# Performance work log

Hardware: AMD Instinct MI355X
Metric: run time of the kernel (lower is better)

## Reference

```python
import jax, jax.numpy as jnp
import numpy as np

NUM_E = 100000
NUM_REL2 = 460  # 2 * num_rel
H = 200
N_EDGES = 1000000
B = 512
RRELU_SLOPE = (1.0 / 8.0 + 1.0 / 3.0) / 2.0  # F.rrelu eval-mode slope
BN_EPS = 1e-5


def setup_inputs() -> dict:
    key = jax.random.key(0)
    ks = jax.random.split(key, 20)
    d = {}
    d["ent_emb"] = jax.random.normal(ks[0], (NUM_E, H), jnp.float32) * 0.1
    d["rel_emb"] = jax.random.normal(ks[1], (NUM_REL2, H), jnp.float32) * 0.1
    d["W_neigh1"] = jax.random.normal(ks[2], (H, H), jnp.float32) * (1.0 / np.sqrt(H))
    d["W_loop1"] = jax.random.normal(ks[3], (H, H), jnp.float32) * (1.0 / np.sqrt(H))
    d["W_neigh2"] = jax.random.normal(ks[4], (H, H), jnp.float32) * (1.0 / np.sqrt(H))
    d["W_loop2"] = jax.random.normal(ks[5], (H, H), jnp.float32) * (1.0 / np.sqrt(H))
    d["gate_theta"] = jax.random.normal(ks[6], (NUM_E, H), jnp.float32) * 0.1
    d["gate_w"] = jax.random.normal(ks[7], (H, 1), jnp.float32) * (1.0 / np.sqrt(H))
    d["gate_b"] = jnp.zeros((1,), jnp.float32)
    d["bn_gamma"] = jnp.ones((3,), jnp.float32)
    d["bn_beta"] = jnp.zeros((3,), jnp.float32)
    d["conv_w"] = jax.random.normal(ks[8], (3,), jnp.float32)
    d["conv_b"] = jnp.zeros((1,), jnp.float32)
    d["freq"] = jax.random.normal(ks[9], (B, H), jnp.float32)
    d["src"] = jax.random.randint(ks[10], (N_EDGES,), 0, NUM_E, jnp.int64)
    d["dst"] = jax.random.randint(ks[11], (N_EDGES,), 0, NUM_E, jnp.int64)
    d["etype"] = jax.random.randint(ks[12], (N_EDGES,), 0, NUM_REL2, jnp.int64)
    d["s_idx"] = jax.random.randint(ks[13], (B,), 0, NUM_E, jnp.int64)
    d["r_idx"] = jax.random.randint(ks[14], (B,), 0, NUM_REL2, jnp.int64)
    return d


def _rrelu(x):
    return jnp.where(x >= 0, x, x * RRELU_SLOPE)


def _union_rgcn_layer(h, rel, W_neigh, W_loop, src, dst):
    # gather -> transform -> scatter (UnionRGCNLayer msg: (h_src + r_etype) @ W_neigh)
    msg = (h[src] + rel) @ W_neigh                      # [E, H]
    agg = jax.ops.segment_sum(msg, dst, num_segments=NUM_E)
    deg = jax.ops.segment_sum(jnp.ones((msg.shape[0],), h.dtype), dst, num_segments=NUM_E)
    agg = agg / jnp.maximum(deg, 1.0)[:, None]          # in-degree norm
    return _rrelu(agg + h @ W_loop)                     # self-loop + activation (dropout off, eval)


def reference(ent_emb, rel_emb, W_neigh1, W_loop1, W_neigh2, W_loop2,
              gate_theta, gate_w, gate_b, bn_gamma, bn_beta, conv_w, conv_b,
              freq, src, dst, etype, s_idx, r_idx):
    rel_per_edge = rel_emb[etype]                       # [E, H]
    # RGCNCell: 2 UnionRGCN layers
    h = _union_rgcn_layer(ent_emb, rel_per_edge, W_neigh1, W_loop1, src, dst)
    h = _union_rgcn_layer(h, rel_per_edge, W_neigh2, W_loop2, src, dst)
    # GatingMechanism: gate = sigmoid(linear(gate_theta[ids])); blend evolved vs static
    gate = jax.nn.sigmoid(gate_theta @ gate_w + gate_b)  # [N, 1]
    h_final = gate * h + (1.0 - gate) * ent_emb          # [N, H]
    # ConvE fusion: stack (entity, rel, frequency) as 3 channels
    e = h_final[s_idx]                                   # [B, H]
    r = rel_emb[r_idx]                                   # [B, H]
    x = jnp.stack([e, r, freq], axis=1)                  # [B, 3, H]
    # BatchNorm1d(3), batch statistics over (B, H) per channel
    mean = jnp.mean(x, axis=(0, 2), keepdims=True)
    var = jnp.var(x, axis=(0, 2), keepdims=True)
    x = (x - mean) * jax.lax.rsqrt(var + BN_EPS)
    x = x * bn_gamma[None, :, None] + bn_beta[None, :, None]
    x = jax.nn.relu(x)
    # Conv1d(3 -> 1, kernel_size=1): weighted channel sum
    q = jnp.einsum('bch,c->bh', x, conv_w) + conv_b      # [B, H]
    # score against all (evolved) entity embeddings
    scores = q @ h_final.T                               # [B, N]
    return scores
```

## Files before the change

### kernel.cpp

```cpp
#include <hip/hip_runtime.h>

#define N_ENT 100000
#define HDIM  200
#define NEDGE 1000000
#define BDIM  512
#define KPAD  416
#define NPAD  208
#define HPAD  224
#define SCAN_TILE 1024
#define SCAN_NB   ((N_ENT + SCAN_TILE - 1)/SCAN_TILE)
#define BN_NB 32

typedef short  short8v __attribute__((ext_vector_type(8)));
typedef float  float4v __attribute__((ext_vector_type(4)));

__device__ __forceinline__ float rrelu_f(float v){
    const float slope = (1.0f/8.0f + 1.0f/3.0f)*0.5f;
    return v >= 0.f ? v : v*slope;
}
__device__ __forceinline__ unsigned short f2bf(float f){
    unsigned int x = __float_as_uint(f);
    unsigned int r = (x + 0x7fffu + ((x >> 16) & 1u)) >> 16;
    return (unsigned short)r;
}
__device__ __forceinline__ float bf2f(unsigned short u){
    return __uint_as_float(((unsigned int)u) << 16);
}

__global__ void hist_k(const int* __restrict__ dst, int* __restrict__ deg){
    int e = blockIdx.x*blockDim.x + threadIdx.x;
    if (e < NEDGE) atomicAdd(&deg[dst[e]], 1);
}

__global__ __launch_bounds__(256) void scan_part_k(const int* __restrict__ deg, int* __restrict__ partial){
    int t = threadIdx.x;
    int base = blockIdx.x*SCAN_TILE + t*4;
    int s = 0;
    if (base + 3 < N_ENT){
        int4 v = *(const int4*)(deg + base);
        s = v.x + v.y + v.z + v.w;
    } else {
        for (int i=0;i<4;i++) if (base+i < N_ENT) s += deg[base+i];
    }
    #pragma unroll
    for (int off=32; off>=1; off>>=1) s += __shfl_xor(s, off);
    __shared__ int ws[4];
    if ((t&63)==0) ws[t>>6] = s;
    __syncthreads();
    if (t==0) partial[blockIdx.x] = ws[0]+ws[1]+ws[2]+ws[3];
}

__global__ void scan_mid_k(int* __restrict__ partial){
    __shared__ int sh[128];
    int t = threadIdx.x;
    int v = (t < SCAN_NB) ? partial[t] : 0;
    sh[t] = v;
    __syncthreads();
    for (int off=1; off<128; off<<=1){
        int u = (t>=off) ? sh[t-off] : 0;
        __syncthreads();
        sh[t] += u;
        __syncthreads();
    }
    if (t < SCAN_NB) partial[t] = sh[t] - v;
}

__global__ __launch_bounds__(256) void scan_fin_k(const int* __restrict__ deg, const int* __restrict__ partial,
        int* __restrict__ row_off, int* __restrict__ fill_pos){
    int t = threadIdx.x;
    int lane = t & 63;
    int base = blockIdx.x*SCAN_TILE + t*4;
    int v0=0,v1=0,v2=0,v3=0;
    if (base+3 < N_ENT){
        int4 v = *(const int4*)(deg + base);
        v0=v.x; v1=v.y; v2=v.z; v3=v.w;
    } else {
        if (base   < N_ENT) v0 = deg[base];
        if (base+1 < N_ENT) v1 = deg[base+1];
        if (base+2 < N_ENT) v2 = deg[base+2];
        if (base+3 < N_ENT) v3 = deg[base+3];
    }
    int s = v0+v1+v2+v3;
    int inc = s;
    #pragma unroll
    for (int off=1; off<64; off<<=1){
        int u = __shfl_up(inc, off);
        if (lane >= off) inc += u;
    }
    __shared__ int wsum[4];
    if (lane==63) wsum[t>>6] = inc;
    __syncthreads();
    int w = t>>6;
    int woff = 0;
    for (int i=0;i<w;i++) woff += wsum[i];
    int exc = partial[blockIdx.x] + woff + inc - s;
    int r0 = exc, r1 = exc+v0, r2 = exc+v0+v1, r3 = exc+v0+v1+v2;
    if (base+3 < N_ENT){
        *(int4*)(row_off+base)  = make_int4(r0,r1,r2,r3);
        *(int4*)(fill_pos+base) = make_int4(r0,r1,r2,r3);
    } else {
        if (base   < N_ENT){ row_off[base]  =r0; fill_pos[base]  =r0; }
        if (base+1 < N_ENT){ row_off[base+1]=r1; fill_pos[base+1]=r1; }
        if (base+2 < N_ENT){ row_off[base+2]=r2; fill_pos[base+2]=r2; }
        if (base+3 < N_ENT){ row_off[base+3]=r3; fill_pos[base+3]=r3; }
    }
    if (blockIdx.x==0 && t==0) row_off[N_ENT] = NEDGE;
}

__global__ void fill_k(const int* __restrict__ src, const int* __restrict__ dst, const int* __restrict__ et,
                       int* __restrict__ fill_pos, int2* __restrict__ cs){
    int e = blockIdx.x*blockDim.x + threadIdx.x;
    if (e < NEDGE){
        int p = atomicAdd(&fill_pos[dst[e]], 1);
        cs[p] = make_int2(src[e], et[e]);
    }
}

__global__ __launch_bounds__(256) void prep_ent_k(const float* __restrict__ ent,
        unsigned short* __restrict__ A1, unsigned short* __restrict__ A2){
    int w = threadIdx.x >> 6, l = threadIdx.x & 63;
    int n = blockIdx.x*4 + w;
    if (l < 50){
        float4 v = *(const float4*)(ent + (size_t)n*HDIM + 4*l);
        ushort4 o; o.x=f2bf(v.x); o.y=f2bf(v.y); o.z=f2bf(v.z); o.w=f2bf(v.w);
        *(ushort4*)(A1 + (size_t)n*KPAD + NPAD + 4*l) = o;
    }
    if (l < 8){
        A1[(size_t)n*KPAD + 200 + l] = 0; A1[(size_t)n*KPAD + 408 + l] = 0;
        A2[(size_t)n*KPAD + 200 + l] = 0; A2[(size_t)n*KPAD + 408 + l] = 0;
    }
}

__global__ void prep_rel_k(const float* __restrict__ rel, unsigned short* __restrict__ relb){
    int i = blockIdx.x*blockDim.x + threadIdx.x;
    if (i < 460*HDIM) relb[i] = f2bf(rel[i]);
}

__global__ void pack_w_k(const float* __restrict__ Wn, const float* __restrict__ Wl,
                         unsigned short* __restrict__ Bpack){
    int i = blockIdx.x*blockDim.x + threadIdx.x;
    if (i >= 13*13*64*8) return;
    int j = i & 7, l = (i >> 3) & 63, rest = i >> 9;
    int f = rest % 13, ks = rest / 13;
    int k = ks*32 + ((l >> 4) << 3) + j;
    int c = f*16 + (l & 15);
    float v = 0.f;
    if (c < HDIM){
        if (k < 200)                  v = Wn[(size_t)k*HDIM + c];
        else if (k >= 208 && k < 408) v = Wl[(size_t)(k-208)*HDIM + c];
    }
    Bpack[i] = f2bf(v);
}

__global__ __launch_bounds__(256) void spmm1_k(unsigned short* __restrict__ Apack,
        const unsigned short* __restrict__ relb,
        const int2* __restrict__ cs,
        const int* __restrict__ row_off,
        unsigned short* __restrict__ relavg){
    int wv = (blockIdx.x*256 + threadIdx.x) >> 6;
    int l = threadIdx.x & 63;
    if (l >= 50) return;
    int beg = row_off[wv], end = row_off[wv+1];
    const int el = 4*l;
    float x0=0.f,x1=0.f,x2=0.f,x3=0.f;
    float r0=0.f,r1=0.f,r2=0.f,r3=0.f;
    int e = beg;
    for (; e+4 <= end; e+=4){
        int2 c0 = cs[e], c1 = cs[e+1], c2 = cs[e+2], c3 = cs[e+3];
        ushort4 xa = *(const ushort4*)(Apack + (size_t)c0.x*KPAD + NPAD + el);
        ushort4 xb = *(const ushort4*)(Apack + (size_t)c1.x*KPAD + NPAD + el);
        ushort4 xc = *(const ushort4*)(Apack + (size_t)c2.x*KPAD + NPAD + el);
        ushort4 xd = *(const ushort4*)(Apack + (size_t)c3.x*KPAD + NPAD + el);
        ushort4 ra = *(const ushort4*)(relb + (size_t)c0.y*HDIM + el);
        ushort4 rb = *(const ushort4*)(relb + (size_t)c1.y*HDIM + el);
        ushort4 rc = *(const ushort4*)(relb + (size_t)c2.y*HDIM + el);
        ushort4 rd = *(const ushort4*)(relb + (size_t)c3.y*HDIM + el);
        x0 += bf2f(xa.x)+bf2f(xb.x)+bf2f(xc.x)+bf2f(xd.x);
        x1 += bf2f(xa.y)+bf2f(xb.y)+bf2f(xc.y)+bf2f(xd.y);
        x2 += bf2f(xa.z)+bf2f(xb.z)+bf2f(xc.z)+bf2f(xd.z);
        x3 += bf2f(xa.w)+bf2f(xb.w)+bf2f(xc.w)+bf2f(xd.w);
        r0 += bf2f(ra.x)+bf2f(rb.x)+bf2f(rc.x)+bf2f(rd.x);
        r1 += bf2f(ra.y)+bf2f(rb.y)+bf2f(rc.y)+bf2f(rd.y);
        r2 += bf2f(ra.z)+bf2f(rb.z)+bf2f(rc.z)+bf2f(rd.z);
        r3 += bf2f(ra.w)+bf2f(rb.w)+bf2f(rc.w)+bf2f(rd.w);
    }
    for (; e<end; e++){
        int2 c0 = cs[e];
        ushort4 xa = *(const ushort4*)(Apack + (size_t)c0.x*KPAD + NPAD + el);
        ushort4 ra = *(const ushort4*)(relb + (size_t)c0.y*HDIM + el);
        x0 += bf2f(xa.x); x1 += bf2f(xa.y); x2 += bf2f(xa.z); x3 += bf2f(xa.w);
        r0 += bf2f(ra.x); r1 += bf2f(ra.y); r2 += bf2f(ra.z); r3 += bf2f(ra.w);
    }
    float id = 1.f / fmaxf((float)(end-beg), 1.f);
    float g0 = r0*id, g1 = r1*id, g2 = r2*id, g3 = r3*id;
    ushort4 rv; rv.x=f2bf(g0); rv.y=f2bf(g1); rv.z=f2bf(g2); rv.w=f2bf(g3);
    *(ushort4*)(relavg + (size_t)wv*HDIM + el) = rv;
    ushort4 o;
    o.x=f2bf(x0*id+g0); o.y=f2bf(x1*id+g1); o.z=f2bf(x2*id+g2); o.w=f2bf(x3*id+g3);
    *(ushort4*)(Apack + (size_t)wv*KPAD + el) = o;
}

__global__ __launch_bounds__(256) void spmm2_k(unsigned short* __restrict__ Apack,
        const unsigned short* __restrict__ relavg,
        const int2* __restrict__ cs,
        const int* __restrict__ row_off){
    int wv = (blockIdx.x*256 + threadIdx.x) >> 6;
    int l = threadIdx.x & 63;
    if (l >= 50) return;
    int beg = row_off[wv], end = row_off[wv+1];
    const int el = 4*l;
    float x0=0.f,x1=0.f,x2=0.f,x3=0.f;
    int e = beg;
    for (; e+4 <= end; e+=4){
        int2 c0 = cs[e], c1 = cs[e+1], c2 = cs[e+2], c3 = cs[e+3];
        ushort4 xa = *(const ushort4*)(Apack + (size_t)c0.x*KPAD + NPAD + el);
        ushort4 xb = *(const ushort4*)(Apack + (size_t)c1.x*KPAD + NPAD + el);
        ushort4 xc = *(const ushort4*)(Apack + (size_t)c2.x*KPAD + NPAD + el);
        ushort4 xd = *(const ushort4*)(Apack + (size_t)c3.x*KPAD + NPAD + el);
        x0 += bf2f(xa.x)+bf2f(xb.x)+bf2f(xc.x)+bf2f(xd.x);
        x1 += bf2f(xa.y)+bf2f(xb.y)+bf2f(xc.y)+bf2f(xd.y);
        x2 += bf2f(xa.z)+bf2f(xb.z)+bf2f(xc.z)+bf2f(xd.z);
        x3 += bf2f(xa.w)+bf2f(xb.w)+bf2f(xc.w)+bf2f(xd.w);
    }
    for (; e<end; e++){
        int2 c0 = cs[e];
        ushort4 xa = *(const ushort4*)(Apack + (size_t)c0.x*KPAD + NPAD + el);
        x0 += bf2f(xa.x); x1 += bf2f(xa.y); x2 += bf2f(xa.z); x3 += bf2f(xa.w);
    }
    float id = 1.f / fmaxf((float)(end-beg), 1.f);
    ushort4 rv = *(const ushort4*)(relavg + (size_t)wv*HDIM + el);
    ushort4 o;
    o.x=f2bf(x0*id+bf2f(rv.x)); o.y=f2bf(x1*id+bf2f(rv.y));
    o.z=f2bf(x2*id+bf2f(rv.z)); o.w=f2bf(x3*id+bf2f(rv.w));
    *(ushort4*)(Apack + (size_t)wv*KPAD + el) = o;
}

__global__ __launch_bounds__(256) void gate_k(const float* __restrict__ th, const float* __restrict__ gw,
                       const float* __restrict__ gb, float* __restrict__ gate){
    int wv = (blockIdx.x*256 + threadIdx.x)>>6;
    int lane = threadIdx.x & 63;
    const float* t = th + (size_t)wv*HDIM;
    float s = t[lane]*gw[lane] + t[64+lane]*gw[64+lane] + t[128+lane]*gw[128+lane];
    if (lane<8) s += t[192+lane]*gw[192+lane];
    #pragma unroll
    for (int off=32; off>=1; off>>=1) s += __shfl_xor(s, off);
    if (lane==0) gate[wv] = 1.f/(1.f + expf(-(s + gb[0])));
}

template<int EPI>
__global__ __launch_bounds__(256,2) void gemm_layer_mfma_k(
        const unsigned short* __restrict__ Apack,
        const unsigned short* __restrict__ Bpack,
        unsigned short* __restrict__ OutB,
        const float* __restrict__ gate, const float* __restrict__ ent){
    __shared__ unsigned short OutS[128*208];
    const int tid = threadIdx.x;
    const int l   = tid & 63;
    const int w   = tid >> 6;
    const int n0  = blockIdx.x * 128;
    const int lr  = l & 15;
    const int lg  = l >> 4;
    int r0 = n0 + w*32 + lr;
    int r1 = r0 + 16;
    int c0 = r0 < N_ENT ? r0 : N_ENT-1;
    int c1 = r1 < N_ENT ? r1 : N_ENT-1;
    const unsigned short* ar0 = Apack + (size_t)c0*KPAD + lg*8;
    const unsigned short* ar1 = Apack + (size_t)c1*KPAD + lg*8;
    float4v acc[2][13];
    #pragma unroll
    for (int f=0; f<13; f++){
        acc[0][f] = (float4v){0.f,0.f,0.f,0.f};
        acc[1][f] = (float4v){0.f,0.f,0.f,0.f};
    }
    short8v a0 = *(const short8v*)(ar0);
    short8v a1 = *(const short8v*)(ar1);
    for (int ks=0; ks<13; ks++){
        short8v na0 = a0, na1 = a1;
        if (ks < 12){
            na0 = *(const short8v*)(ar0 + (ks+1)*32);
            na1 = *(const short8v*)(ar1 + (ks+1)*32);
        }
        const unsigned short* bp = Bpack + ((size_t)(ks*13)*64 + l)*8;
        #pragma unroll
        for (int f=0; f<13; f++){
            short8v b = *(const short8v*)(bp + (size_t)f*512);
            acc[0][f] = __builtin_amdgcn_mfma_f32_16x16x32_bf16(a0, b, acc[0][f], 0, 0, 0);
            acc[1][f] = __builtin_amdgcn_mfma_f32_16x16x32_bf16(a1, b, acc[1][f], 0, 0, 0);
        }
        a0 = na0; a1 = na1;
    }
    #pragma unroll
    for (int f=0; f<13; f++){
        int c = f*16 + lr;
        if (c < HDIM){
            #pragma unroll
            for (int j=0; j<4; j++){
                OutS[(w*32 + lg*4 + j)*208 + c]      = f2bf(rrelu_f(acc[0][f][j]));
                OutS[(w*32 + 16 + lg*4 + j)*208 + c] = f2bf(rrelu_f(acc[1][f][j]));
            }
        }
    }
    __syncthreads();
    for (int i = tid; i < 128*25; i += 256){
        int r = i/25, seg = i - r*25;
        int n = n0 + r;
        if (n >= N_ENT) continue;
        short8v v = *(const short8v*)(&OutS[r*208 + seg*8]);
        if (EPI == 2){
            float g = gate[n];
            const float4* ef = (const float4*)(ent + (size_t)n*HDIM + seg*8);
            float4 e0 = ef[0], e1 = ef[1];
            float ev[8] = {e0.x,e0.y,e0.z,e0.w,e1.x,e1.y,e1.z,e1.w};
            short8v o;
            #pragma unroll
            for (int j=0; j<8; j++){
                float x = g*bf2f((unsigned short)v[j]) + (1.f-g)*ev[j];
                o[j] = (short)f2bf(x);
            }
            *(short8v*)(OutB + (size_t)n*HPAD + seg*8) = o;
        } else {
            *(short8v*)(OutB + (size_t)n*KPAD + NPAD + seg*8) = v;
        }
    }
}

__global__ void zero_hfb_pad_k(unsigned short* __restrict__ hfb){
    int i = blockIdx.x*blockDim.x + threadIdx.x;
    if (i >= N_ENT*24) return;
    int n = i / 24, c = 200 + (i - n*24);
    hfb[(size_t)n*HPAD + c] = 0;
}

__global__ __launch_bounds__(256) void bn_part_k(const unsigned short* __restrict__ hfb,
        const float* __restrict__ rel, const float* __restrict__ freq,
        const int* __restrict__ s_idx, const int* __restrict__ r_idx,
        float* __restrict__ bnpart){
    int t = threadIdx.x;
    float acc[6] = {0,0,0,0,0,0};
    for (int i = blockIdx.x*256 + t; i < BDIM*HDIM; i += BN_NB*256){
        int b = i/HDIM, h = i - b*HDIM;
        float e = bf2f(hfb[(size_t)s_idx[b]*HPAD + h]);
        float r = rel[(size_t)r_idx[b]*HDIM + h];
        float f = freq[i];
        acc[0]+=e; acc[1]+=e*e; acc[2]+=r; acc[3]+=r*r; acc[4]+=f; acc[5]+=f*f;
    }
    __shared__ float red[4][6];
    #pragma unroll
    for (int c=0;c<6;c++){
        float s = acc[c];
        #pragma unroll
        for (int off=32; off>=1; off>>=1) s += __shfl_xor(s, off);
        if ((t&63)==0) red[t>>6][c] = s;
    }
    __syncthreads();
    if (t==0){
        #pragma unroll
        for (int c=0;c<6;c++)
            bnpart[blockIdx.x*6+c] = red[0][c]+red[1][c]+red[2][c]+red[3][c];
    }
}

__global__ void bn_fin_k(const float* __restrict__ bnpart, float* __restrict__ bnp){
    int t = threadIdx.x;
    if (t < 3){
        float s=0.f, q=0.f;
        for (int b=0;b<BN_NB;b++){ s += bnpart[b*6+2*t]; q += bnpart[b*6+2*t+1]; }
        const float inv = 1.f/(float)(BDIM*HDIM);
        float mean = s*inv;
        float var  = q*inv - mean*mean;
        bnp[t]   = mean;
        bnp[3+t] = rsqrtf(var + 1e-5f);
    }
}

__global__ void qt_k(const unsigned short* __restrict__ hfb, const float* __restrict__ rel,
        const float* __restrict__ freq, const int* __restrict__ s_idx, const int* __restrict__ r_idx,
        const float* __restrict__ gamma, const float* __restrict__ beta,
        const float* __restrict__ convw, const float* __restrict__ convb,
        const float* __restrict__ bnp, unsigned short* __restrict__ qb){
    int i = blockIdx.x*blockDim.x + threadIdx.x;
    if (i >= BDIM*HPAD) return;
    int b = i/HPAD, h = i - b*HPAD;
    if (h >= HDIM){ qb[i] = 0; return; }
    float x0 = bf2f(hfb[(size_t)s_idx[b]*HPAD + h]);
    float x1 = rel[(size_t)r_idx[b]*HDIM + h];
    float x2 = freq[(size_t)b*HDIM + h];
    float v0 = fmaxf((x0-bnp[0])*bnp[3]*gamma[0] + beta[0], 0.f);
    float v1 = fmaxf((x1-bnp[1])*bnp[4]*gamma[1] + beta[1], 0.f);
    float v2 = fmaxf((x2-bnp[2])*bnp[5]*gamma[2] + beta[2], 0.f);
    float q = v0*convw[0] + v1*convw[1] + v2*convw[2] + convb[0];
    qb[(size_t)b*HPAD + h] = f2bf(q);
}

__global__ __launch_bounds__(256,2) void scores_mfma_k(
        const unsigned short* __restrict__ hfb,
        const unsigned short* __restrict__ qb,
        float* __restrict__ out){
    const int tid = threadIdx.x;
    const int l   = tid & 63;
    const int w   = tid >> 6;
    const int lr  = l & 15;
    const int lg  = l >> 4;
    const int n0  = blockIdx.x * 64;
    float4v acc[8][4];
    #pragma unroll
    for (int bf=0; bf<8; bf++)
        #pragma unroll
        for (int nf=0; nf<4; nf++) acc[bf][nf] = (float4v){0,0,0,0};
    const unsigned short* hptr[4];
    #pragma unroll
    for (int nf=0; nf<4; nf++){
        int n = n0 + nf*16 + lr;
        if (n >= N_ENT) n = N_ENT-1;
        hptr[nf] = hfb + (size_t)n*HPAD + lg*8;
    }
    const unsigned short* qrow = qb + (size_t)(w*128 + lr)*HPAD + lg*8;
    for (int ks=0; ks<7; ks++){
        short8v hv[4];
        #pragma unroll
        for (int nf=0; nf<4; nf++) hv[nf] = *(const short8v*)(hptr[nf] + ks*32);
        #pragma unroll
        for (int bf=0; bf<8; bf++){
            short8v q = *(const short8v*)(qrow + (size_t)bf*16*HPAD + ks*32);
            #pragma unroll
            for (int nf=0; nf<4; nf++)
                acc[bf][nf] = __builtin_amdgcn_mfma_f32_16x16x32_bf16(q, hv[nf], acc[bf][nf], 0, 0, 0);
        }
    }
    #pragma unroll
    for (int bf=0; bf<8; bf++){
        int b = w*128 + bf*16 + lg*4;
        #pragma unroll
        for (int nf=0; nf<4; nf++){
            int n = n0 + nf*16 + lr;
            if (n >= N_ENT) continue;
            #pragma unroll
            for (int j=0; j<4; j++){
                out[(size_t)(b+j)*N_ENT + n] = acc[bf][nf][j];
            }
        }
    }
}

extern "C" void kernel_launch(void* const* d_in, const int* in_sizes, int n_in,
                              void* d_out, int out_size, void* d_ws, size_t ws_size,
                              hipStream_t stream) {
    const float* ent    = (const float*)d_in[0];
    const float* rel    = (const float*)d_in[1];
    const float* Wn1    = (const float*)d_in[2];
    const float* Wl1    = (const float*)d_in[3];
    const float* Wn2    = (const float*)d_in[4];
    const float* Wl2    = (const float*)d_in[5];
    const float* gtheta = (const float*)d_in[6];
    const float* gw     = (const float*)d_in[7];
    const float* gb     = (const float*)d_in[8];
    const float* gamma  = (const float*)d_in[9];
    const float* beta   = (const float*)d_in[10];
    const float* convw  = (const float*)d_in[11];
    const float* convb  = (const float*)d_in[12];
    const float* freq   = (const float*)d_in[13];
    const int*   src    = (const int*)d_in[14];
    const int*   dst    = (const int*)d_in[15];
    const int*   etype  = (const int*)d_in[16];
    const int*   s_idx  = (const int*)d_in[17];
    const int*   r_idx  = (const int*)d_in[18];
    float* out = (float*)d_out;

    char* ws = (char*)d_ws;
    size_t off = 0;
    auto alloc = [&](size_t bytes)->char*{
        char* p = ws + off;
        off += (bytes + 511) & ~(size_t)511;
        return p;
    };
    int*   deg      = (int*)alloc((size_t)N_ENT*4);
    int*   row_off  = (int*)alloc((size_t)(N_ENT+1)*4);
    int*   fill_pos = (int*)alloc((size_t)N_ENT*4);
    int*   partial  = (int*)alloc((size_t)SCAN_NB*4);
    int2*  cs       = (int2*)alloc((size_t)NEDGE*8);
    unsigned short* A1     = (unsigned short*)alloc((size_t)N_ENT*KPAD*2);
    unsigned short* A2     = (unsigned short*)alloc((size_t)N_ENT*KPAD*2);
    unsigned short* relavg = (unsigned short*)alloc((size_t)N_ENT*HDIM*2);
    unsigned short* relb   = (unsigned short*)alloc((size_t)460*HDIM*2);
    unsigned short* Bp1    = (unsigned short*)alloc((size_t)13*13*64*8*2);
    unsigned short* Bp2    = (unsigned short*)alloc((size_t)13*13*64*8*2);
    unsigned short* qb     = (unsigned short*)alloc((size_t)BDIM*HPAD*2);
    float* gate   = (float*)alloc((size_t)N_ENT*4);
    float* bnpart = (float*)alloc((size_t)BN_NB*6*4);
    float* bnp    = (float*)alloc(64);
    unsigned short* hfb = A1;

    hipMemsetAsync(deg, 0, (size_t)N_ENT*4, stream);

    const int EB = (NEDGE + 255)/256;
    hist_k<<<EB,256,0,stream>>>(dst, deg);
    scan_part_k<<<SCAN_NB,256,0,stream>>>(deg, partial);
    scan_mid_k<<<1,128,0,stream>>>(partial);
    scan_fin_k<<<SCAN_NB,256,0,stream>>>(deg, partial, row_off, fill_pos);
    fill_k<<<EB,256,0,stream>>>(src, dst, etype, fill_pos, cs);

    prep_ent_k<<<N_ENT/4,256,0,stream>>>(ent, A1, A2);
    prep_rel_k<<<(460*HDIM+255)/256,256,0,stream>>>(rel, relb);
    pack_w_k<<<(13*13*64*8+255)/256,256,0,stream>>>(Wn1, Wl1, Bp1);
    pack_w_k<<<(13*13*64*8+255)/256,256,0,stream>>>(Wn2, Wl2, Bp2);

    const int NWB = N_ENT/4;
    const int GTB = (N_ENT + 127)/128;

    spmm1_k<<<NWB,256,0,stream>>>(A1, relb, cs, row_off, relavg);
    gemm_layer_mfma_k<1><<<GTB,256,0,stream>>>(A1, Bp1, A2, nullptr, nullptr);

    zero_hfb_pad_k<<<(N_ENT*24+255)/256,256,0,stream>>>(hfb);
    gate_k<<<NWB,256,0,stream>>>(gtheta, gw, gb, gate);

    spmm2_k<<<NWB,256,0,stream>>>(A2, relavg, cs, row_off);
    gemm_layer_mfma_k<2><<<GTB,256,0,stream>>>(A2, Bp2, hfb, gate, ent);

    bn_part_k<<<BN_NB,256,0,stream>>>(hfb, rel, freq, s_idx, r_idx, bnpart);
    bn_fin_k<<<1,64,0,stream>>>(bnpart, bnp);
    qt_k<<<(BDIM*HPAD+255)/256,256,0,stream>>>(hfb, rel, freq, s_idx, r_idx, gamma, beta, convw, convb, bnp, qb);

    scores_mfma_k<<<(N_ENT+63)/64,256,0,stream>>>(hfb, qb, out);

    (void)in_sizes; (void)n_in; (void)out_size; (void)ws_size;
}
```

Measured before the change: 627.8 us.

## Split packed activation buffer into separate padded X/P buffers and fuse prep kernels

New measurement: 574.3 us. -8.5%, faster.

```diff
diff --git a/kernel.cpp b/kernel.cpp
--- a/kernel.cpp
+++ b/kernel.cpp
@@ -4,12 +4,14 @@
 #define HDIM  200
 #define NEDGE 1000000
 #define BDIM  512
-#define KPAD  416
-#define NPAD  208
-#define HPAD  224
+#define PITCH 224
+#define NSEG  28
+#define NF    13
 #define SCAN_TILE 1024
 #define SCAN_NB   ((N_ENT + SCAN_TILE - 1)/SCAN_TILE)
 #define BN_NB 32
+#define RELB_ELEMS (460*PITCH)
+#define BP_ELEMS   (14*NF*64*8)
 
 typedef short  short8v __attribute__((ext_vector_type(8)));
 typedef float  float4v __attribute__((ext_vector_type(4)));
@@ -25,6 +27,73 @@
 }
 __device__ __forceinline__ float bf2f(unsigned short u){
     return __uint_as_float(((unsigned int)u) << 16);
+}
+
+__device__ __forceinline__ void pack_b(int b, const float* __restrict__ Wn,
+        const float* __restrict__ Wl, unsigned short* __restrict__ Bp){
+    int i = b*1024 + threadIdx.x*4;
+    #pragma unroll
+    for (int k=0;k<4;k++){
+        int idx = i+k;
+        if (idx < BP_ELEMS){
+            int j = idx & 7, l = (idx >> 3) & 63, rest = idx >> 9;
+            int f = rest % NF, ks = rest / NF;
+            int kk = ks*32 + ((l >> 4) << 3) + j;
+            int c  = f*16 + (l & 15);
+            float v = 0.f;
+            if (c < HDIM){
+                if (kk < 200)                  v = Wn[(size_t)kk*HDIM + c];
+                else if (kk >= 224 && kk < 424) v = Wl[(size_t)(kk-224)*HDIM + c];
+            }
+            Bp[idx] = f2bf(v);
+        }
+    }
+}
+
+__global__ __launch_bounds__(256) void init_k(const float* __restrict__ ent,
+        const float* __restrict__ rel,
+        const float* __restrict__ Wn1, const float* __restrict__ Wl1,
+        const float* __restrict__ Wn2, const float* __restrict__ Wl2,
+        int* __restrict__ deg, unsigned short* __restrict__ relb,
+        unsigned short* __restrict__ Bp1, unsigned short* __restrict__ Bp2,
+        unsigned short* __restrict__ Xbuf1){
+    int b = blockIdx.x;
+    if (b < 98){
+        int i = b*1024 + threadIdx.x*4;
+        if (i+3 < N_ENT) *(int4*)(deg+i) = make_int4(0,0,0,0);
+        else { for (int k=0;k<4;k++) if (i+k < N_ENT) deg[i+k]=0; }
+        return;
+    }
+    b -= 98;
+    if (b < 101){
+        int i = b*1024 + threadIdx.x*4;
+        #pragma unroll
+        for (int k=0;k<4;k++){
+            int idx = i+k;
+            if (idx < RELB_ELEMS){
+                int r = idx / PITCH, c = idx - r*PITCH;
+                relb[idx] = (c < HDIM) ? f2bf(rel[(size_t)r*HDIM + c]) : 0;
+            }
+        }
+        return;
+    }
+    b -= 101;
+    if (b < 91){ pack_b(b, Wn1, Wl1, Bp1); return; }
+    b -= 91;
+    if (b < 91){ pack_b(b, Wn2, Wl2, Bp2); return; }
+    b -= 91;
+    int w = threadIdx.x >> 6, l = threadIdx.x & 63;
+    if (l >= 56) return;
+    int n = b*4 + w;
+    int el = 4*l;
+    ushort4 o;
+    if (el < HDIM){
+        float4 v = *(const float4*)(ent + (size_t)n*HDIM + el);
+        o.x=f2bf(v.x); o.y=f2bf(v.y); o.z=f2bf(v.z); o.w=f2bf(v.w);
+    } else {
+        o.x=o.y=o.z=o.w=0;
+    }
+    *(ushort4*)(Xbuf1 + (size_t)n*PITCH + el) = o;
 }
 
 __global__ void hist_k(const int* __restrict__ dst, int* __restrict__ deg){
@@ -116,50 +185,15 @@
     }
 }
 
-__global__ __launch_bounds__(256) void prep_ent_k(const float* __restrict__ ent,
-        unsigned short* __restrict__ A1, unsigned short* __restrict__ A2){
-    int w = threadIdx.x >> 6, l = threadIdx.x & 63;
-    int n = blockIdx.x*4 + w;
-    if (l < 50){
-        float4 v = *(const float4*)(ent + (size_t)n*HDIM + 4*l);
-        ushort4 o; o.x=f2bf(v.x); o.y=f2bf(v.y); o.z=f2bf(v.z); o.w=f2bf(v.w);
-        *(ushort4*)(A1 + (size_t)n*KPAD + NPAD + 4*l) = o;
-    }
-    if (l < 8){
-        A1[(size_t)n*KPAD + 200 + l] = 0; A1[(size_t)n*KPAD + 408 + l] = 0;
-        A2[(size_t)n*KPAD + 200 + l] = 0; A2[(size_t)n*KPAD + 408 + l] = 0;
-    }
-}
-
-__global__ void prep_rel_k(const float* __restrict__ rel, unsigned short* __restrict__ relb){
-    int i = blockIdx.x*blockDim.x + threadIdx.x;
-    if (i < 460*HDIM) relb[i] = f2bf(rel[i]);
-}
-
-__global__ void pack_w_k(const float* __restrict__ Wn, const float* __restrict__ Wl,
-                         unsigned short* __restrict__ Bpack){
-    int i = blockIdx.x*blockDim.x + threadIdx.x;
-    if (i >= 13*13*64*8) return;
-    int j = i & 7, l = (i >> 3) & 63, rest = i >> 9;
-    int f = rest % 13, ks = rest / 13;
-    int k = ks*32 + ((l >> 4) << 3) + j;
-    int c = f*16 + (l & 15);
-    float v = 0.f;
-    if (c < HDIM){
-        if (k < 200)                  v = Wn[(size_t)k*HDIM + c];
-        else if (k >= 208 && k < 408) v = Wl[(size_t)(k-208)*HDIM + c];
-    }
-    Bpack[i] = f2bf(v);
-}
-
-__global__ __launch_bounds__(256) void spmm1_k(unsigned short* __restrict__ Apack,
+__global__ __launch_bounds__(256) void spmm1_k(const unsigned short* __restrict__ X,
+        unsigned short* __restrict__ P,
         const unsigned short* __restrict__ relb,
         const int2* __restrict__ cs,
         const int* __restrict__ row_off,
         unsigned short* __restrict__ relavg){
     int wv = (blockIdx.x*256 + threadIdx.x) >> 6;
     int l = threadIdx.x & 63;
-    if (l >= 50) return;
+    if (l >= 56) return;
     int beg = row_off[wv], end = row_off[wv+1];
     const int el = 4*l;
     float x0=0.f,x1=0.f,x2=0.f,x3=0.f;
@@ -167,14 +201,14 @@
     int e = beg;
     for (; e+4 <= end; e+=4){
         int2 c0 = cs[e], c1 = cs[e+1], c2 = cs[e+2], c3 = cs[e+3];
-        ushort4 xa = *(const ushort4*)(Apack + (size_t)c0.x*KPAD + NPAD + el);
-        ushort4 xb = *(const ushort4*)(Apack + (size_t)c1.x*KPAD + NPAD + el);
-        ushort4 xc = *(const ushort4*)(Apack + (size_t)c2.x*KPAD + NPAD + el);
-        ushort4 xd = *(const ushort4*)(Apack + (size_t)c3.x*KPAD + NPAD + el);
-        ushort4 ra = *(const ushort4*)(relb + (size_t)c0.y*HDIM + el);
-        ushort4 rb = *(const ushort4*)(relb + (size_t)c1.y*HDIM + el);
-        ushort4 rc = *(const ushort4*)(relb + (size_t)c2.y*HDIM + el);
-        ushort4 rd = *(const ushort4*)(relb + (size_t)c3.y*HDIM + el);
+        ushort4 xa = *(const ushort4*)(X + (size_t)c0.x*PITCH + el);
+        ushort4 xb = *(const ushort4*)(X + (size_t)c1.x*PITCH + el);
+        ushort4 xc = *(const ushort4*)(X + (size_t)c2.x*PITCH + el);
+        ushort4 xd = *(const ushort4*)(X + (size_t)c3.x*PITCH + el);
+        ushort4 ra = *(const ushort4*)(relb + (size_t)c0.y*PITCH + el);
+        ushort4 rb = *(const ushort4*)(relb + (size_t)c1.y*PITCH + el);
+        ushort4 rc = *(const ushort4*)(relb + (size_t)c2.y*PITCH + el);
+        ushort4 rd = *(const ushort4*)(relb + (size_t)c3.y*PITCH + el);
         x0 += bf2f(xa.x)+bf2f(xb.x)+bf2f(xc.x)+bf2f(xd.x);
         x1 += bf2f(xa.y)+bf2f(xb.y)+bf2f(xc.y)+bf2f(xd.y);
         x2 += bf2f(xa.z)+bf2f(xb.z)+bf2f(xc.z)+bf2f(xd.z);
@@ -186,37 +220,38 @@
     }
     for (; e<end; e++){
         int2 c0 = cs[e];
-        ushort4 xa = *(const ushort4*)(Apack + (size_t)c0.x*KPAD + NPAD + el);
-        ushort4 ra = *(const ushort4*)(relb + (size_t)c0.y*HDIM + el);
+        ushort4 xa = *(const ushort4*)(X + (size_t)c0.x*PITCH + el);
+        ushort4 ra = *(const ushort4*)(relb + (size_t)c0.y*PITCH + el);
         x0 += bf2f(xa.x); x1 += bf2f(xa.y); x2 += bf2f(xa.z); x3 += bf2f(xa.w);
         r0 += bf2f(ra.x); r1 += bf2f(ra.y); r2 += bf2f(ra.z); r3 += bf2f(ra.w);
     }
     float id = 1.f / fmaxf((float)(end-beg), 1.f);
     float g0 = r0*id, g1 = r1*id, g2 = r2*id, g3 = r3*id;
     ushort4 rv; rv.x=f2bf(g0); rv.y=f2bf(g1); rv.z=f2bf(g2); rv.w=f2bf(g3);
-    *(ushort4*)(relavg + (size_t)wv*HDIM + el) = rv;
+    *(ushort4*)(relavg + (size_t)wv*PITCH + el) = rv;
     ushort4 o;
     o.x=f2bf(x0*id+g0); o.y=f2bf(x1*id+g1); o.z=f2bf(x2*id+g2); o.w=f2bf(x3*id+g3);
-    *(ushort4*)(Apack + (size_t)wv*KPAD + el) = o;
-}
-
-__global__ __launch_bounds__(256) void spmm2_k(unsigned short* __restrict__ Apack,
+    *(ushort4*)(P + (size_t)wv*PITCH + el) = o;
+}
+
+__global__ __launch_bounds__(256) void spmm2_k(const unsigned short* __restrict__ X,
+        unsigned short* __restrict__ P,
         const unsigned short* __restrict__ relavg,
         const int2* __restrict__ cs,
         const int* __restrict__ row_off){
     int wv = (blockIdx.x*256 + threadIdx.x) >> 6;
     int l = threadIdx.x & 63;
-    if (l >= 50) return;
+    if (l >= 56) return;
     int beg = row_off[wv], end = row_off[wv+1];
     const int el = 4*l;
     float x0=0.f,x1=0.f,x2=0.f,x3=0.f;
     int e = beg;
     for (; e+4 <= end; e+=4){
         int2 c0 = cs[e], c1 = cs[e+1], c2 = cs[e+2], c3 = cs[e+3];
-        ushort4 xa = *(const ushort4*)(Apack + (size_t)c0.x*KPAD + NPAD + el);
-        ushort4 xb = *(const ushort4*)(Apack + (size_t)c1.x*KPAD + NPAD + el);
-        ushort4 xc = *(const ushort4*)(Apack + (size_t)c2.x*KPAD + NPAD + el);
-        ushort4 xd = *(const ushort4*)(Apack + (size_t)c3.x*KPAD + NPAD + el);
+        ushort4 xa = *(const ushort4*)(X + (size_t)c0.x*PITCH + el);
+        ushort4 xb = *(const ushort4*)(X + (size_t)c1.x*PITCH + el);
+        ushort4 xc = *(const ushort4*)(X + (size_t)c2.x*PITCH + el);
+        ushort4 xd = *(const ushort4*)(X + (size_t)c3.x*PITCH + el);
         x0 += bf2f(xa.x)+bf2f(xb.x)+bf2f(xc.x)+bf2f(xd.x);
         x1 += bf2f(xa.y)+bf2f(xb.y)+bf2f(xc.y)+bf2f(xd.y);
         x2 += bf2f(xa.z)+bf2f(xb.z)+bf2f(xc.z)+bf2f(xd.z);
@@ -224,15 +259,15 @@
     }
     for (; e<end; e++){
         int2 c0 = cs[e];
-        ushort4 xa = *(const ushort4*)(Apack + (size_t)c0.x*KPAD + NPAD + el);
+        ushort4 xa = *(const ushort4*)(X + (size_t)c0.x*PITCH + el);
         x0 += bf2f(xa.x); x1 += bf2f(xa.y); x2 += bf2f(xa.z); x3 += bf2f(xa.w);
     }
     float id = 1.f / fmaxf((float)(end-beg), 1.f);
-    ushort4 rv = *(const ushort4*)(relavg + (size_t)wv*HDIM + el);
+    ushort4 rv = *(const ushort4*)(relavg + (size_t)wv*PITCH + el);
     ushort4 o;
     o.x=f2bf(x0*id+bf2f(rv.x)); o.y=f2bf(x1*id+bf2f(rv.y));
     o.z=f2bf(x2*id+bf2f(rv.z)); o.w=f2bf(x3*id+bf2f(rv.w));
-    *(ushort4*)(Apack + (size_t)wv*KPAD + el) = o;
+    *(ushort4*)(P + (size_t)wv*PITCH + el) = o;
 }
 
 __global__ __launch_bounds__(256) void gate_k(const float* __restrict__ th, const float* __restrict__ gw,
@@ -249,11 +284,12 @@
 
 template<int EPI>
 __global__ __launch_bounds__(256,2) void gemm_layer_mfma_k(
-        const unsigned short* __restrict__ Apack,
+        const unsigned short* __restrict__ Pb,
+        const unsigned short* __restrict__ Xb,
         const unsigned short* __restrict__ Bpack,
         unsigned short* __restrict__ OutB,
         const float* __restrict__ gate, const float* __restrict__ ent){
-    __shared__ unsigned short OutS[128*208];
+    __shared__ unsigned short OutS[128*PITCH];
     const int tid = threadIdx.x;
     const int l   = tid & 63;
     const int w   = tid >> 6;
@@ -264,71 +300,68 @@
     int r1 = r0 + 16;
     int c0 = r0 < N_ENT ? r0 : N_ENT-1;
     int c1 = r1 < N_ENT ? r1 : N_ENT-1;
-    const unsigned short* ar0 = Apack + (size_t)c0*KPAD + lg*8;
-    const unsigned short* ar1 = Apack + (size_t)c1*KPAD + lg*8;
-    float4v acc[2][13];
-    #pragma unroll
-    for (int f=0; f<13; f++){
+    float4v acc[2][NF];
+    #pragma unroll
+    for (int f=0; f<NF; f++){
         acc[0][f] = (float4v){0.f,0.f,0.f,0.f};
         acc[1][f] = (float4v){0.f,0.f,0.f,0.f};
     }
-    short8v a0 = *(const short8v*)(ar0);
-    short8v a1 = *(const short8v*)(ar1);
-    for (int ks=0; ks<13; ks++){
-        short8v na0 = a0, na1 = a1;
-        if (ks < 12){
-            na0 = *(const short8v*)(ar0 + (ks+1)*32);
-            na1 = *(const short8v*)(ar1 + (ks+1)*32);
-        }
-        const unsigned short* bp = Bpack + ((size_t)(ks*13)*64 + l)*8;
-        #pragma unroll
-        for (int f=0; f<13; f++){
-            short8v b = *(const short8v*)(bp + (size_t)f*512);
-            acc[0][f] = __builtin_amdgcn_mfma_f32_16x16x32_bf16(a0, b, acc[0][f], 0, 0, 0);
-            acc[1][f] = __builtin_amdgcn_mfma_f32_16x16x32_bf16(a1, b, acc[1][f], 0, 0, 0);
-        }
-        a0 = na0; a1 = na1;
-    }
-    #pragma unroll
-    for (int f=0; f<13; f++){
+    #pragma unroll 1
+    for (int sec=0; sec<2; sec++){
+        const unsigned short* base = sec ? Xb : Pb;
+        const unsigned short* a0p = base + (size_t)c0*PITCH + lg*8;
+        const unsigned short* a1p = base + (size_t)c1*PITCH + lg*8;
+        const unsigned short* bp0 = Bpack + (((size_t)(sec*7*NF))*64 + l)*8;
+        for (int ks=0; ks<7; ks++){
+            short8v a0 = *(const short8v*)(a0p + ks*32);
+            short8v a1 = *(const short8v*)(a1p + ks*32);
+            const unsigned short* bp = bp0 + (size_t)ks*NF*512;
+            #pragma unroll
+            for (int f=0; f<NF; f++){
+                short8v b = *(const short8v*)(bp + (size_t)f*512);
+                acc[0][f] = __builtin_amdgcn_mfma_f32_16x16x32_bf16(a0, b, acc[0][f], 0, 0, 0);
+                acc[1][f] = __builtin_amdgcn_mfma_f32_16x16x32_bf16(a1, b, acc[1][f], 0, 0, 0);
+            }
+        }
+    }
+    #pragma unroll
+    for (int f=0; f<NF; f++){
         int c = f*16 + lr;
         if (c < HDIM){
             #pragma unroll
             for (int j=0; j<4; j++){
-                OutS[(w*32 + lg*4 + j)*208 + c]      = f2bf(rrelu_f(acc[0][f][j]));
-                OutS[(w*32 + 16 + lg*4 + j)*208 + c] = f2bf(rrelu_f(acc[1][f][j]));
+                OutS[(w*32 + lg*4 + j)*PITCH + c]      = f2bf(rrelu_f(acc[0][f][j]));
+                OutS[(w*32 + 16 + lg*4 + j)*PITCH + c] = f2bf(rrelu_f(acc[1][f][j]));
             }
         }
     }
     __syncthreads();
-    for (int i = tid; i < 128*25; i += 256){
-        int r = i/25, seg = i - r*25;
+    for (int i = tid; i < 128*NSEG; i += 256){
+        int r = i/NSEG, seg = i - r*NSEG;
         int n = n0 + r;
         if (n >= N_ENT) continue;
-        short8v v = *(const short8v*)(&OutS[r*208 + seg*8]);
-        if (EPI == 2){
-            float g = gate[n];
-            const float4* ef = (const float4*)(ent + (size_t)n*HDIM + seg*8);
-            float4 e0 = ef[0], e1 = ef[1];
-            float ev[8] = {e0.x,e0.y,e0.z,e0.w,e1.x,e1.y,e1.z,e1.w};
-            short8v o;
+        short8v o;
+        if (seg >= 25){
             #pragma unroll
-            for (int j=0; j<8; j++){
-                float x = g*bf2f((unsigned short)v[j]) + (1.f-g)*ev[j];
-                o[j] = (short)f2bf(x);
+            for (int j=0;j<8;j++) o[j]=0;
+        } else {
+            short8v v = *(const short8v*)(&OutS[r*PITCH + seg*8]);
+            if (EPI == 2){
+                float g = gate[n];
+                const float4* ef = (const float4*)(ent + (size_t)n*HDIM + seg*8);
+                float4 e0 = ef[0], e1 = ef[1];
+                float ev[8] = {e0.x,e0.y,e0.z,e0.w,e1.x,e1.y,e1.z,e1.w};
+                #pragma unroll
+                for (int j=0; j<8; j++){
+                    float x = g*bf2f((unsigned short)v[j]) + (1.f-g)*ev[j];
+                    o[j] = (short)f2bf(x);
+                }
+            } else {
+                o = v;
             }
-            *(short8v*)(OutB + (size_t)n*HPAD + seg*8) = o;
-        } else {
-            *(short8v*)(OutB + (size_t)n*KPAD + NPAD + seg*8) = v;
-        }
-    }
-}
-
-__global__ void zero_hfb_pad_k(unsigned short* __restrict__ hfb){
-    int i = blockIdx.x*blockDim.x + threadIdx.x;
-    if (i >= N_ENT*24) return;
-    int n = i / 24, c = 200 + (i - n*24);
-    hfb[(size_t)n*HPAD + c] = 0;
+        }
+        *(short8v*)(OutB + (size_t)n*PITCH + seg*8) = o;
+    }
 }
 
 __global__ __launch_bounds__(256) void bn_part_k(const unsigned short* __restrict__ hfb,
@@ -339,7 +372,7 @@
     float acc[6] = {0,0,0,0,0,0};
     for (int i = blockIdx.x*256 + t; i < BDIM*HDIM; i += BN_NB*256){
         int b = i/HDIM, h = i - b*HDIM;
-        float e = bf2f(hfb[(size_t)s_idx[b]*HPAD + h]);
+        float e = bf2f(hfb[(size_t)s_idx[b]*PITCH + h]);
         float r = rel[(size_t)r_idx[b]*HDIM + h];
         float f = freq[i];
         acc[0]+=e; acc[1]+=e*e; acc[2]+=r; acc[3]+=r*r; acc[4]+=f; acc[5]+=f*f;
@@ -379,17 +412,17 @@
         const float* __restrict__ convw, const float* __restrict__ convb,
         const float* __restrict__ bnp, unsigned short* __restrict__ qb){
     int i = blockIdx.x*blockDim.x + threadIdx.x;
-    if (i >= BDIM*HPAD) return;
-    int b = i/HPAD, h = i - b*HPAD;
+    if (i >= BDIM*PITCH) return;
+    int b = i/PITCH, h = i - b*PITCH;
     if (h >= HDIM){ qb[i] = 0; return; }
-    float x0 = bf2f(hfb[(size_t)s_idx[b]*HPAD + h]);
+    float x0 = bf2f(hfb[(size_t)s_idx[b]*PITCH + h]);
     float x1 = rel[(size_t)r_idx[b]*HDIM + h];
     float x2 = freq[(size_t)b*HDIM + h];
     float v0 = fmaxf((x0-bnp[0])*bnp[3]*gamma[0] + beta[0], 0.f);
     float v1 = fmaxf((x1-bnp[1])*bnp[4]*gamma[1] + beta[1], 0.f);
     float v2 = fmaxf((x2-bnp[2])*bnp[5]*gamma[2] + beta[2], 0.f);
     float q = v0*convw[0] + v1*convw[1] + v2*convw[2] + convb[0];
-    qb[(size_t)b*HPAD + h] = f2bf(q);
+    qb[(size_t)b*PITCH + h] = f2bf(q);
 }
 
 __global__ __launch_bounds__(256,2) void scores_mfma_k(
@@ -412,16 +445,16 @@
     for (int nf=0; nf<4; nf++){
         int n = n0 + nf*16 + lr;
         if (n >= N_ENT) n = N_ENT-1;
-        hptr[nf] = hfb + (size_t)n*HPAD + lg*8;
-    }
-    const unsigned short* qrow = qb + (size_t)(w*128 + lr)*HPAD + lg*8;
+        hptr[nf] = hfb + (size_t)n*PITCH + lg*8;
+    }
+    const unsigned short* qrow = qb + (size_t)(w*128 + lr)*PITCH + lg*8;
     for (int ks=0; ks<7; ks++){
         short8v hv[4];
         #pragma unroll
         for (int nf=0; nf<4; nf++) hv[nf] = *(const short8v*)(hptr[nf] + ks*32);
         #pragma unroll
         for (int bf=0; bf<8; bf++){
-            short8v q = *(const short8v*)(qrow + (size_t)bf*16*HPAD + ks*32);
+            short8v q = *(const short8v*)(qrow + (size_t)bf*16*PITCH + ks*32);
             #pragma unroll
             for (int nf=0; nf<4; nf++)
                 acc[bf][nf] = __builtin_amdgcn_mfma_f32_16x16x32_bf16(q, hv[nf], acc[bf][nf], 0, 0, 0);
@@ -478,47 +511,43 @@
     int*   fill_pos = (int*)alloc((size_t)N_ENT*4);
     int*   partial  = (int*)alloc((size_t)SCAN_NB*4);
     int2*  cs       = (int2*)alloc((size_t)NEDGE*8);
-    unsigned short* A1     = (unsigned short*)alloc((size_t)N_ENT*KPAD*2);
-    unsigned short* A2     = (unsigned short*)alloc((size_t)N_ENT*KPAD*2);
-    unsigned short* relavg = (unsigned short*)alloc((size_t)N_ENT*HDIM*2);
-    unsigned short* relb   = (unsigned short*)alloc((size_t)460*HDIM*2);
-    unsigned short* Bp1    = (unsigned short*)alloc((size_t)13*13*64*8*2);
-    unsigned short* Bp2    = (unsigned short*)alloc((size_t)13*13*64*8*2);
-    unsigned short* qb     = (unsigned short*)alloc((size_t)BDIM*HPAD*2);
+    unsigned short* Xbuf1  = (unsigned short*)alloc((size_t)N_ENT*PITCH*2);
+    unsigned short* Pbuf1  = (unsigned short*)alloc((size_t)N_ENT*PITCH*2);
+    unsigned short* Xbuf2  = (unsigned short*)alloc((size_t)N_ENT*PITCH*2);
+    unsigned short* Pbuf2  = (unsigned short*)alloc((size_t)N_ENT*PITCH*2);
+    unsigned short* relavg = (unsigned short*)alloc((size_t)N_ENT*PITCH*2);
+    unsigned short* relb   = (unsigned short*)alloc((size_t)RELB_ELEMS*2);
+    unsigned short* Bp1    = (unsigned short*)alloc((size_t)BP_ELEMS*2);
+    unsigned short* Bp2    = (unsigned short*)alloc((size_t)BP_ELEMS*2);
+    unsigned short* qb     = (unsigned short*)alloc((size_t)BDIM*PITCH*2);
     float* gate   = (float*)alloc((size_t)N_ENT*4);
     float* bnpart = (float*)alloc((size_t)BN_NB*6*4);
     float* bnp    = (float*)alloc(64);
-    unsigned short* hfb = A1;
-
-    hipMemsetAsync(deg, 0, (size_t)N_ENT*4, stream);
+    unsigned short* hfb = Xbuf1;
 
     const int EB = (NEDGE + 255)/256;
+    const int INIT_NB = 98 + 101 + 91 + 91 + N_ENT/4;
+
+    init_k<<<INIT_NB,256,0,stream>>>(ent, rel, Wn1, Wl1, Wn2, Wl2, deg, relb, Bp1, Bp2, Xbuf1);
     hist_k<<<EB,256,0,stream>>>(dst, deg);
     scan_part_k<<<SCAN_NB,256,0,stream>>>(deg, partial);
     scan_mid_k<<<1,128,0,stream>>>(partial);
     scan_fin_k<<<SCAN_NB,256,0,stream>>>(deg, partial, row_off, fill_pos);
     fill_k<<<EB,256,0,stream>>>(src, dst, etype, fill_pos, cs);
-
-    prep_ent_k<<<N_ENT/4,256,0,stream>>>(ent, A1, A2);
-    prep_rel_k<<<(460*HDIM+255)/256,256,0,stream>>>(rel, relb);
-    pack_w_k<<<(13*13*64*8+255)/256,256,0,stream>>>(Wn1, Wl1, Bp1);
-    pack_w_k<<<(13*13*64*8+255)/256,256,0,stream>>>(Wn2, Wl2, Bp2);
+    gate_k<<<N_ENT/4,256,0,stream>>>(gtheta, gw, gb, gate);
 
     const int NWB = N_ENT/4;
     const int GTB = (N_ENT + 127)/128;
 
-    spmm1_k<<<NWB,256,0,stream>>>(A1, relb, cs, row_off, relavg);
-    gemm_layer_mfma_k<1><<<GTB,256,0,stream>>>(A1, Bp1, A2, nullptr, nullptr);
-
-    zero_hfb_pad_k<<<(N_ENT*24+255)/256,256,0,stream>>>(hfb);
-    gate_k<<<NWB,256,0,stream>>>(gtheta, gw, gb, gate);
-
-    spmm2_k<<<NWB,256,0,stream>>>(A2, relavg, cs, row_off);
-    gemm_layer_mfma_k<2><<<GTB,256,0,stream>>>(A2, Bp2, hfb, gate, ent);
+    spmm1_k<<<NWB,256,0,stream>>>(Xbuf1, Pbuf1, relb, cs, row_off, relavg);
+    gemm_layer_mfma_k<1><<<GTB,256,0,stream>>>(Pbuf1, Xbuf1, Bp1, Xbuf2, nullptr, nullptr);
+
+    spmm2_k<<<NWB,256,0,stream>>>(Xbuf2, Pbuf2, relavg, cs, row_off);
+    gemm_layer_mfma_k<2><<<GTB,256,0,stream>>>(Pbuf2, Xbuf2, Bp2, hfb, gate, ent);
 
     bn_part_k<<<BN_NB,256,0,stream>>>(hfb, rel, freq, s_idx, r_idx, bnpart);
     bn_fin_k<<<1,64,0,stream>>>(bnpart, bnp);
-    qt_k<<<(BDIM*HPAD+255)/256,256,0,stream>>>(hfb, rel, freq, s_idx, r_idx, gamma, beta, convw, convb, bnp, qb);
+    qt_k<<<(BDIM*PITCH+255)/256,256,0,stream>>>(hfb, rel, freq, s_idx, r_idx, gamma, beta, convw, convb, bnp, qb);
 
     scores_mfma_k<<<(N_ENT+63)/64,256,0,stream>>>(hfb, qb, out);
 
```
